# Kernel tuning notes

Hardware: AMD Instinct MI355X
Metric: run time of the kernel (lower is better)

## Reference

```python
import jax, jax.numpy as jnp
import numpy as np

B, C, N, K, COUT = 8, 128, 10000, 16, 256


def setup_inputs() -> dict:
    key = jax.random.key(0)
    ks = jax.random.split(key, 8)
    x = jax.random.normal(ks[0], (B, C, N, 1), dtype=jnp.float32)
    edge_index = jax.random.randint(ks[1], (2, B, N, K), 0, N)
    s1 = 1.0 / np.sqrt(C)
    W1 = jax.random.uniform(ks[2], (C, C), jnp.float32, -s1, s1)   # nn1 1x1 conv weight
    b1 = jax.random.uniform(ks[3], (C,), jnp.float32, -s1, s1)
    Wp = jax.random.uniform(ks[4], (C, C), jnp.float32, -s1, s1)   # nn_pooling Linear
    bp = jax.random.uniform(ks[5], (C,), jnp.float32, -s1, s1)
    s2 = 1.0 / np.sqrt(2 * C)
    W2 = jax.random.uniform(ks[6], (COUT, 2 * C), jnp.float32, -s2, s2)  # nn2 1x1 conv
    b2 = jax.random.uniform(ks[7], (COUT,), jnp.float32, -s2, s2)
    return dict(x=x, edge_index=edge_index, W1=W1, b1=b1, Wp=Wp, bp=bp, W2=W2, b2=b2)


def reference(x, edge_index, W1, b1, Wp, bp, W2, b2):
    b, c, n, _ = x.shape
    k = edge_index.shape[-1]
    # nn1: 1x1 conv (channel mix) + ReLU -> [B,C,N,1]
    h = jax.nn.relu(jnp.einsum('bcns,dc->bdns', x, W1) + b1[None, :, None, None])
    # batched_index_select: gather neighbor features along vertex dim -> [B,C,N,K]
    hn = h[:, :, :, 0]                              # [B,C,N]
    idx = edge_index[0].reshape(b, 1, n * k)        # broadcast over C
    xj = jnp.take_along_axis(hn, idx, axis=2).reshape(b, c, n, k)
    # nn_pooling: Linear over channel dim + ReLU (transpose(1,3) in torch == act on C)
    xj = jax.nn.relu(jnp.einsum('bcnk,dc->bdnk', xj, Wp) + bp[None, :, None, None])
    # max-pool over neighbors, keepdim -> [B,C,N,1]
    xj = jnp.max(xj, axis=-1, keepdims=True)
    # concat along channels, nn2: 1x1 conv + ReLU -> [B,COUT,N,1]
    cat = jnp.concatenate([h, xj], axis=1)
    out = jax.nn.relu(jnp.einsum('bcns,dc->bdns', cat, W2) + b2[None, :, None, None])
    return out
```

## Files before the change

### kernel.cpp

```cpp
#include <hip/hip_runtime.h>

#define NODES 10000
#define BATCH 8
#define CH    128
#define KNB   16
#define CO    256

typedef __bf16 bf16x8 __attribute__((ext_vector_type(8)));
typedef float  f32x4  __attribute__((ext_vector_type(4)));

__device__ __forceinline__ unsigned short f2bf(float f) {
  unsigned u = __float_as_uint(f);
  u = (u + 0x7FFFu + ((u >> 16) & 1u)) >> 16;
  return (unsigned short)u;
}

__device__ __forceinline__ unsigned pkmax(unsigned a, unsigned b) {
  unsigned d;
  asm("v_pk_max_u16 %0, %1, %2" : "=v"(d) : "v"(a), "v"(b));
  return d;
}
__device__ __forceinline__ uint4 pkmax4(uint4 a, uint4 b) {
  a.x = pkmax(a.x, b.x); a.y = pkmax(a.y, b.y);
  a.z = pkmax(a.z, b.z); a.w = pkmax(a.w, b.w);
  return a;
}
__device__ __forceinline__ bf16x8 asbf8(uint4 u) {
  union { uint4 u; bf16x8 b; } c; c.u = u; return c.b;
}

__device__ __forceinline__ void gload_lds16(const void* g, void* l) {
  __builtin_amdgcn_global_load_lds(
      (const __attribute__((address_space(1))) unsigned int*)g,
      (__attribute__((address_space(3))) unsigned int*)l, 16, 0, 0);
}

__device__ __forceinline__ void lds_barrier() {
  asm volatile("s_waitcnt lgkmcnt(0)" ::: "memory");
  __builtin_amdgcn_sched_barrier(0);
  __builtin_amdgcn_s_barrier();
}

__global__ __launch_bounds__(256) void prep(
    const float* __restrict__ W1, const float* __restrict__ Wp,
    const float* __restrict__ W2,
    unsigned short* __restrict__ W1b, unsigned short* __restrict__ Wpb,
    unsigned short* __restrict__ W2b)
{
  int i = blockIdx.x * 256 + threadIdx.x;
  const float* src; unsigned short* dst; int off;
  if (i < 4096)      { src = W1; dst = W1b; off = i; }
  else if (i < 8192) { src = Wp; dst = Wpb; off = i - 4096; }
  else               { src = W2; dst = W2b; off = i - 8192; }
  float4 v = ((const float4*)src)[off];
  ushort4 o;
  o.x = f2bf(v.x); o.y = f2bf(v.y); o.z = f2bf(v.z); o.w = f2bf(v.w);
  ((ushort4*)dst)[off] = o;
}

__device__ __forceinline__ void hz_load_x(
    f32x4 (&xa)[4][2], const float* __restrict__ X, int n0, int t)
{
#pragma unroll
  for (int rep = 0; rep < 4; ++rep) {
    int flat = t + rep * 256;
    int c2 = flat >> 4, n4 = flat & 15;
    int c  = c2 * 2;
    int gn = n0 + n4 * 4;
    f32x4 a0 = (f32x4){0.f,0.f,0.f,0.f}, a1 = a0;
    if (gn < NODES) {
      a0 = *(const f32x4*)(X + (size_t)c * NODES + gn);
      a1 = *(const f32x4*)(X + (size_t)(c + 1) * NODES + gn);
    }
    xa[rep][0] = a0; xa[rep][1] = a1;
  }
}

__device__ __forceinline__ void hz_write_buf(
    const f32x4 (&xa)[4][2], unsigned short* buf, int t)
{
  char* BtB = (char*)buf;
#pragma unroll
  for (int rep = 0; rep < 4; ++rep) {
    int flat = t + rep * 256;
    int c2 = flat >> 4, n4 = flat & 15;
#pragma unroll
    for (int i = 0; i < 4; ++i) {
      int nn = n4 * 4 + i;
      unsigned pk = (unsigned)f2bf(xa[rep][0][i])
                  | ((unsigned)f2bf(xa[rep][1][i]) << 16);
      int phys = nn * 256 + (((c2 >> 2) ^ (nn & 7)) << 4) + ((c2 & 3) << 2);
      *(unsigned*)(BtB + phys) = pk;
    }
  }
}

__device__ __forceinline__ void hz_compute(
    const unsigned short* buf, unsigned short* Ht, unsigned short* Zt,
    const uint4 (&af)[4][4], const uint4 (&af2)[4][4],
    const float* __restrict__ b1, const float* __restrict__ bp,
    unsigned short* __restrict__ h_t, unsigned short* __restrict__ z_t,
    size_t nb, int n0, int t, int w, int lm, int q)
{
  const char* BtB = (const char*)buf;
  char* HtB = (char*)Ht;
  char* ZtB = (char*)Zt;
  const int d0  = (w & 1) * 64;
  const int nbw = (w >> 1) * 32;

  f32x4 acc[4][2];
#pragma unroll
  for (int dt = 0; dt < 4; ++dt)
#pragma unroll
    for (int nt = 0; nt < 2; ++nt) acc[dt][nt] = (f32x4){0.f,0.f,0.f,0.f};

#pragma unroll
  for (int kt = 0; kt < 4; ++kt)
#pragma unroll
    for (int nt = 0; nt < 2; ++nt) {
      int nl = nbw + nt * 16 + lm;
      int chunk = kt * 4 + q;
      int phys = nl * 256 + ((chunk ^ (nl & 7)) << 4);
      bf16x8 bb = asbf8(*(const uint4*)(BtB + phys));
#pragma unroll
      for (int dt = 0; dt < 4; ++dt)
        acc[dt][nt] = __builtin_amdgcn_mfma_f32_16x16x32_bf16(
            asbf8(af[dt][kt]), bb, acc[dt][nt], 0, 0, 0);
    }

#pragma unroll
  for (int dt = 0; dt < 4; ++dt) {
    int dbase = d0 + dt * 16 + q * 4;
    float4 bi = *(const float4*)(b1 + dbase);
    float bv[4] = {bi.x, bi.y, bi.z, bi.w};
#pragma unroll
    for (int nt = 0; nt < 2; ++nt) {
      int nl = nbw + nt * 16 + lm;
      ushort4 o;
      o.x = f2bf(fmaxf(acc[dt][nt][0] + bv[0], 0.f));
      o.y = f2bf(fmaxf(acc[dt][nt][1] + bv[1], 0.f));
      o.z = f2bf(fmaxf(acc[dt][nt][2] + bv[2], 0.f));
      o.w = f2bf(fmaxf(acc[dt][nt][3] + bv[3], 0.f));
      int chunk = dbase >> 3;
      int phys  = nl * 256 + ((chunk ^ (nl & 7)) << 4) + ((q & 1) << 3);
      *(ushort4*)(HtB + phys) = o;
    }
  }

  lds_barrier();

  {
    int nl = t >> 2;
    int gn = n0 + nl;
#pragma unroll
    for (int rep = 0; rep < 4; ++rep) {
      int g = (t & 3) + rep * 4;
      int phys = nl * 256 + ((g ^ (nl & 7)) << 4);
      uint4 v = *(const uint4*)(HtB + phys);
      if (gn < NODES)
        *(uint4*)((char*)h_t + (nb + (size_t)gn) * 256 + g * 16) = v;
    }
  }

#pragma unroll
  for (int dt = 0; dt < 4; ++dt)
#pragma unroll
    for (int nt = 0; nt < 2; ++nt) acc[dt][nt] = (f32x4){0.f,0.f,0.f,0.f};

#pragma unroll
  for (int kt = 0; kt < 4; ++kt)
#pragma unroll
    for (int nt = 0; nt < 2; ++nt) {
      int nl = nbw + nt * 16 + lm;
      int chunk = kt * 4 + q;
      int phys = nl * 256 + ((chunk ^ (nl & 7)) << 4);
      bf16x8 bb = asbf8(*(const uint4*)(HtB + phys));
#pragma unroll
      for (int dt = 0; dt < 4; ++dt)
        acc[dt][nt] = __builtin_amdgcn_mfma_f32_16x16x32_bf16(
            asbf8(af2[dt][kt]), bb, acc[dt][nt], 0, 0, 0);
    }

#pragma unroll
  for (int dt = 0; dt < 4; ++dt) {
    int dbase = d0 + dt * 16 + q * 4;
    float4 bi = *(const float4*)(bp + dbase);
    float bv[4] = {bi.x, bi.y, bi.z, bi.w};
#pragma unroll
    for (int nt = 0; nt < 2; ++nt) {
      int nl = nbw + nt * 16 + lm;
      ushort4 o;
      o.x = f2bf(fmaxf(acc[dt][nt][0] + bv[0], 0.f));
      o.y = f2bf(fmaxf(acc[dt][nt][1] + bv[1], 0.f));
      o.z = f2bf(fmaxf(acc[dt][nt][2] + bv[2], 0.f));
      o.w = f2bf(fmaxf(acc[dt][nt][3] + bv[3], 0.f));
      int chunk = dbase >> 3;
      int phys  = nl * 256 + ((chunk ^ (nl & 7)) << 4) + ((q & 1) << 3);
      *(ushort4*)(ZtB + phys) = o;
    }
  }

  lds_barrier();

  {
    int nl = t >> 2;
    int gn = n0 + nl;
#pragma unroll
    for (int rep = 0; rep < 4; ++rep) {
      int g = (t & 3) + rep * 4;
      int phys = nl * 256 + ((g ^ (nl & 7)) << 4);
      uint4 v = *(const uint4*)(ZtB + phys);
      if (gn < NODES)
        *(uint4*)((char*)z_t + (nb + (size_t)gn) * 256 + g * 16) = v;
    }
  }
}

__global__ __launch_bounds__(256) void fused_hz(
    const unsigned short* __restrict__ W1b, const float* __restrict__ b1,
    const unsigned short* __restrict__ Wpb, const float* __restrict__ bp,
    const float* __restrict__ x,
    unsigned short* __restrict__ h_t, unsigned short* __restrict__ z_t)
{
  const int bid = blockIdx.x;
  const int b   = bid & 7;
  const int g   = bid >> 3;
  const int t   = threadIdx.x;
  const int lane = t & 63, w = t >> 6;
  const int lm = lane & 15, q = lane >> 4;
  const size_t nb = (size_t)b * NODES;
  const float* X = x + (size_t)b * CH * NODES;

  __shared__ __align__(16) unsigned short bufA[64 * 128];
  __shared__ __align__(16) unsigned short bufB[64 * 128];
  __shared__ __align__(16) unsigned short Ht[64 * 128];
  __shared__ __align__(16) unsigned short Zt[64 * 128];

  const int d0 = (w & 1) * 64;

  uint4 af[4][4], af2[4][4];
#pragma unroll
  for (int dt = 0; dt < 4; ++dt)
#pragma unroll
    for (int kt = 0; kt < 4; ++kt) {
      af[dt][kt]  = *(const uint4*)(W1b + (d0 + dt*16 + lm) * CH + kt*32 + q*8);
      af2[dt][kt] = *(const uint4*)(Wpb + (d0 + dt*16 + lm) * CH + kt*32 + q*8);
    }

  const int n0_0 = g * 64;
  const int n0_1 = (g + 64) * 64;
  const int n0_2 = (g + 128) * 64;
  const bool has2 = (g + 128) < 157;

  f32x4 xa[4][2];

  hz_load_x(xa, X, n0_0, t);
  hz_write_buf(xa, bufA, t);
  __syncthreads();

  hz_load_x(xa, X, n0_1, t);
  hz_compute(bufA, Ht, Zt, af, af2, b1, bp, h_t, z_t, nb, n0_0, t, w, lm, q);
  hz_write_buf(xa, bufB, t);
  __syncthreads();

  if (has2) {
    hz_load_x(xa, X, n0_2, t);
    hz_compute(bufB, Ht, Zt, af, af2, b1, bp, h_t, z_t, nb, n0_1, t, w, lm, q);
    hz_write_buf(xa, bufA, t);
    __syncthreads();
    hz_compute(bufA, Ht, Zt, af, af2, b1, bp, h_t, z_t, nb, n0_2, t, w, lm, q);
  } else {
    hz_compute(bufB, Ht, Zt, af, af2, b1, bp, h_t, z_t, nb, n0_1, t, w, lm, q);
  }
}

__global__ __launch_bounds__(256) void gmax_kernel(
    const unsigned short* __restrict__ z_t, const int* __restrict__ e0,
    unsigned short* __restrict__ zm)
{
  const int bid = blockIdx.x;
  const int b   = bid & 7;
  const int n0  = (bid >> 3) * 64;
  const int t   = threadIdx.x;
  const int nl  = t >> 2, c = t & 3;
  const int gn  = n0 + nl;
  if (gn >= NODES) return;

  const int* ip = e0 + ((size_t)b * NODES + gn) * KNB;
  int4 iv0 = *(const int4*)(ip);
  int4 iv1 = *(const int4*)(ip + 4);
  int4 iv2 = *(const int4*)(ip + 8);
  int4 iv3 = *(const int4*)(ip + 12);
  int idx[16] = {iv0.x, iv0.y, iv0.z, iv0.w,
                 iv1.x, iv1.y, iv1.z, iv1.w,
                 iv2.x, iv2.y, iv2.z, iv2.w,
                 iv3.x, iv3.y, iv3.z, iv3.w};

  const char* Z = (const char*)(z_t + (size_t)b * NODES * CH) + c * 16;
  uint4 m[4];
#pragma unroll
  for (int cg = 0; cg < 4; ++cg) m[cg] = make_uint4(0u, 0u, 0u, 0u);

#pragma unroll
  for (int k = 0; k < KNB; ++k) {
    const char* p = Z + (size_t)idx[k] * (CH * 2);
#pragma unroll
    for (int cg = 0; cg < 4; ++cg)
      m[cg] = pkmax4(m[cg], *(const uint4*)(p + cg * 64));
  }

  char* O = (char*)(zm + ((size_t)b * NODES + gn) * CH) + c * 16;
#pragma unroll
  for (int cg = 0; cg < 4; ++cg)
    *(uint4*)(O + cg * 64) = m[cg];
}

__device__ __forceinline__ void og_stage(
    unsigned short* buf, const unsigned short* __restrict__ h_t,
    const unsigned short* __restrict__ zm, size_t nb, int n0, int w, int lane)
{
#pragma unroll
  for (int rep = 0; rep < 8; ++rep) {
    const int row0 = w * 2 + rep * 8;
    const int nl = row0 + (lane >> 5);
    const int l  = (lane & 31) ^ (nl & 7);
    int gn = n0 + nl; if (gn > NODES - 1) gn = NODES - 1;
    const unsigned short* src = (l < 16)
        ? h_t + (nb + (size_t)gn) * CH + l * 8
        : zm  + (nb + (size_t)gn) * CH + (l - 16) * 8;
    gload_lds16(src, (char*)buf + row0 * 512);
  }
  __builtin_amdgcn_sched_barrier(0);
}

__device__ __forceinline__ void og_mfma(
    f32x4 (&acc)[4][4], const unsigned short* buf,
    const uint4 (&af)[8][4], int lm, int q)
{
  const char* catB = (const char*)buf;
#pragma unroll
  for (int dt = 0; dt < 4; ++dt)
#pragma unroll
    for (int nt = 0; nt < 4; ++nt) acc[dt][nt] = (f32x4){0.f, 0.f, 0.f, 0.f};
#pragma unroll
  for (int kt = 0; kt < 8; ++kt)
#pragma unroll
    for (int nt = 0; nt < 4; ++nt) {
      int nl = nt * 16 + lm;
      int chunk = kt * 4 + q;
      int phys = nl * 512 + ((chunk ^ (nl & 7)) << 4);
      bf16x8 bb = asbf8(*(const uint4*)(catB + phys));
#pragma unroll
      for (int dt = 0; dt < 4; ++dt)
        acc[dt][nt] = __builtin_amdgcn_mfma_f32_16x16x32_bf16(
            asbf8(af[kt][dt]), bb, acc[dt][nt], 0, 0, 0);
    }
}

__device__ __forceinline__ void og_epi(
    const f32x4 (&acc)[4][4], const float* __restrict__ b2,
    float* __restrict__ out, int b, int n0, int w, int lm, int q)
{
  const int d0 = w * 64;
#pragma unroll
  for (int dt = 0; dt < 4; ++dt) {
    int dbase = d0 + dt * 16 + q * 4;
    float4 bi = *(const float4*)(b2 + dbase);
    float bv[4] = {bi.x, bi.y, bi.z, bi.w};
#pragma unroll
    for (int nt = 0; nt < 4; ++nt) {
      int gn = n0 + nt * 16 + lm;
      if (gn < NODES) {
        float* op = out + ((size_t)(b * CO + dbase) * NODES) + gn;
#pragma unroll
        for (int r = 0; r < 4; ++r)
          op[(size_t)r * NODES] = fmaxf(acc[dt][nt][r] + bv[r], 0.f);
      }
    }
  }
}

__global__ __launch_bounds__(256) void out_gemm(
    const unsigned short* __restrict__ h_t, const unsigned short* __restrict__ zm,
    const unsigned short* __restrict__ W2b, const float* __restrict__ b2,
    float* __restrict__ out)
{
  const int bid = blockIdx.x;
  const int b   = bid & 7;
  const int g   = bid >> 3;
  const int t   = threadIdx.x;
  const int lane = t & 63, w = t >> 6;
  const int lm = lane & 15, q = lane >> 4;
  const size_t nb = (size_t)b * NODES;

  __shared__ __align__(16) unsigned short bufA[64 * 256];
  __shared__ __align__(16) unsigned short bufB[64 * 256];

  const int d0 = w * 64;
  uint4 af[8][4];
#pragma unroll
  for (int kt = 0; kt < 8; ++kt)
#pragma unroll
    for (int dt = 0; dt < 4; ++dt)
      af[kt][dt] = *(const uint4*)(W2b + (d0 + dt*16 + lm) * CO + kt*32 + q*8);

  const int n0_0 = g * 64;
  const int n0_1 = (g + 64) * 64;
  const int n0_2 = (g + 128) * 64;
  const bool has2 = (g + 128) < 157;

  f32x4 acc[4][4];

  og_stage(bufA, h_t, zm, nb, n0_0, w, lane);
  asm volatile("s_waitcnt vmcnt(0) lgkmcnt(0)" ::: "memory");
  __builtin_amdgcn_sched_barrier(0);
  __builtin_amdgcn_s_barrier();

  og_stage(bufB, h_t, zm, nb, n0_1, w, lane);
  og_mfma(acc, bufA, af, lm, q);
  asm volatile("s_waitcnt vmcnt(0) lgkmcnt(0)" ::: "memory");
  __builtin_amdgcn_sched_barrier(0);
  __builtin_amdgcn_s_barrier();

  if (has2) {
    og_stage(bufA, h_t, zm, nb, n0_2, w, lane);
    og_epi(acc, b2, out, b, n0_0, w, lm, q);
    og_mfma(acc, bufB, af, lm, q);
    asm volatile("s_waitcnt vmcnt(56) lgkmcnt(0)" ::: "memory");
    __builtin_amdgcn_sched_barrier(0);
    __builtin_amdgcn_s_barrier();
    og_epi(acc, b2, out, b, n0_1, w, lm, q);
    og_mfma(acc, bufA, af, lm, q);
    og_epi(acc, b2, out, b, n0_2, w, lm, q);
  } else {
    og_epi(acc, b2, out, b, n0_0, w, lm, q);
    og_mfma(acc, bufB, af, lm, q);
    og_epi(acc, b2, out, b, n0_1, w, lm, q);
  }
}

extern "C" void kernel_launch(void* const* d_in, const int* in_sizes, int n_in,
                              void* d_out, int out_size, void* d_ws, size_t ws_size,
                              hipStream_t stream) {
  const float* x  = (const float*)d_in[0];
  const int*   ei = (const int*)d_in[1];
  const float* W1 = (const float*)d_in[2];
  const float* b1 = (const float*)d_in[3];
  const float* Wp = (const float*)d_in[4];
  const float* bp = (const float*)d_in[5];
  const float* W2 = (const float*)d_in[6];
  const float* b2 = (const float*)d_in[7];
  float* out = (float*)d_out;

  unsigned short* ws  = (unsigned short*)d_ws;
  unsigned short* h_t = ws;
  unsigned short* z_t = h_t + (size_t)BATCH * NODES * CH;
  unsigned short* W1b = z_t + (size_t)BATCH * NODES * CH;
  unsigned short* Wpb = W1b + CH * CH;
  unsigned short* W2b = Wpb + CH * CH;
  unsigned short* zm  = W2b + CO * 2 * CH;

  prep<<<96, 256, 0, stream>>>(W1, Wp, W2, W1b, Wpb, W2b);

  const int NT = (NODES + 63) / 64;
  fused_hz<<<512, 256, 0, stream>>>(W1b, b1, Wpb, bp, x, h_t, z_t);
  gmax_kernel<<<BATCH * NT, 256, 0, stream>>>(z_t, ei, zm);
  out_gemm<<<512, 256, 0, stream>>>(h_t, zm, W2b, b2, out);
}
```

Measured before the change: 195.0 us.

## Split fused_hz into two-tile blocks and reuse input LDS buffer for Z staging

Each fused_hz block now handles two consecutive 64-node tiles instead of up to three strided tiles, and the grid grows to cover all tiles (8×79 blocks). The separate Zt shared buffer is dropped: the Z output is staged in the input tile buffer once it has been consumed, cutting shared memory per block from 64KB to 48KB. The goal is more resident blocks per CU and less serial work per block, improving latency hiding for the memory-bound first stage. In exchange, each block gets less software pipelining of x loads, and reusing the buffer depends on every wave having finished reading it before it is overwritten.

After: 201.7 us. 3.4% more time.

```diff
diff --git a/kernel.cpp b/kernel.cpp
--- a/kernel.cpp
+++ b/kernel.cpp
@@ -96,15 +96,15 @@
 }
 
 __device__ __forceinline__ void hz_compute(
-    const unsigned short* buf, unsigned short* Ht, unsigned short* Zt,
+    unsigned short* buf,
+    unsigned short* Ht,
     const uint4 (&af)[4][4], const uint4 (&af2)[4][4],
     const float* __restrict__ b1, const float* __restrict__ bp,
     unsigned short* __restrict__ h_t, unsigned short* __restrict__ z_t,
     size_t nb, int n0, int t, int w, int lm, int q)
 {
-  const char* BtB = (const char*)buf;
+  char* BtB = (char*)buf;
   char* HtB = (char*)Ht;
-  char* ZtB = (char*)Zt;
   const int d0  = (w & 1) * 64;
   const int nbw = (w >> 1) * 32;
 
@@ -196,7 +196,7 @@
       o.w = f2bf(fmaxf(acc[dt][nt][3] + bv[3], 0.f));
       int chunk = dbase >> 3;
       int phys  = nl * 256 + ((chunk ^ (nl & 7)) << 4) + ((q & 1) << 3);
-      *(ushort4*)(ZtB + phys) = o;
+      *(ushort4*)(BtB + phys) = o;
     }
   }
 
@@ -209,7 +209,7 @@
     for (int rep = 0; rep < 4; ++rep) {
       int g = (t & 3) + rep * 4;
       int phys = nl * 256 + ((g ^ (nl & 7)) << 4);
-      uint4 v = *(const uint4*)(ZtB + phys);
+      uint4 v = *(const uint4*)(BtB + phys);
       if (gn < NODES)
         *(uint4*)((char*)z_t + (nb + (size_t)gn) * 256 + g * 16) = v;
     }
@@ -224,7 +224,7 @@
 {
   const int bid = blockIdx.x;
   const int b   = bid & 7;
-  const int g   = bid >> 3;
+  const int p   = bid >> 3;
   const int t   = threadIdx.x;
   const int lane = t & 63, w = t >> 6;
   const int lm = lane & 15, q = lane >> 4;
@@ -234,7 +234,6 @@
   __shared__ __align__(16) unsigned short bufA[64 * 128];
   __shared__ __align__(16) unsigned short bufB[64 * 128];
   __shared__ __align__(16) unsigned short Ht[64 * 128];
-  __shared__ __align__(16) unsigned short Zt[64 * 128];
 
   const int d0 = (w & 1) * 64;
 
@@ -247,10 +246,9 @@
       af2[dt][kt] = *(const uint4*)(Wpb + (d0 + dt*16 + lm) * CH + kt*32 + q*8);
     }
 
-  const int n0_0 = g * 64;
-  const int n0_1 = (g + 64) * 64;
-  const int n0_2 = (g + 128) * 64;
-  const bool has2 = (g + 128) < 157;
+  const int n0_0 = p * 128;
+  const int n0_1 = n0_0 + 64;
+  const bool has1 = n0_1 < NODES;
 
   f32x4 xa[4][2];
 
@@ -258,19 +256,14 @@
   hz_write_buf(xa, bufA, t);
   __syncthreads();
 
-  hz_load_x(xa, X, n0_1, t);
-  hz_compute(bufA, Ht, Zt, af, af2, b1, bp, h_t, z_t, nb, n0_0, t, w, lm, q);
-  hz_write_buf(xa, bufB, t);
-  __syncthreads();
-
-  if (has2) {
-    hz_load_x(xa, X, n0_2, t);
-    hz_compute(bufB, Ht, Zt, af, af2, b1, bp, h_t, z_t, nb, n0_1, t, w, lm, q);
-    hz_write_buf(xa, bufA, t);
+  if (has1) {
+    hz_load_x(xa, X, n0_1, t);
+    hz_compute(bufA, Ht, af, af2, b1, bp, h_t, z_t, nb, n0_0, t, w, lm, q);
+    hz_write_buf(xa, bufB, t);
     __syncthreads();
-    hz_compute(bufA, Ht, Zt, af, af2, b1, bp, h_t, z_t, nb, n0_2, t, w, lm, q);
+    hz_compute(bufB, Ht, af, af2, b1, bp, h_t, z_t, nb, n0_1, t, w, lm, q);
   } else {
-    hz_compute(bufB, Ht, Zt, af, af2, b1, bp, h_t, z_t, nb, n0_1, t, w, lm, q);
+    hz_compute(bufA, Ht, af, af2, b1, bp, h_t, z_t, nb, n0_0, t, w, lm, q);
   }
 }
 
@@ -463,7 +456,8 @@
   prep<<<96, 256, 0, stream>>>(W1, Wp, W2, W1b, Wpb, W2b);
 
   const int NT = (NODES + 63) / 64;
-  fused_hz<<<512, 256, 0, stream>>>(W1b, b1, Wpb, bp, x, h_t, z_t);
+  const int NP = (NT + 1) / 2;
+  fused_hz<<<BATCH * NP, 256, 0, stream>>>(W1b, b1, Wpb, bp, x, h_t, z_t);
   gmax_kernel<<<BATCH * NT, 256, 0, stream>>>(z_t, ei, zm);
   out_gemm<<<512, 256, 0, stream>>>(h_t, zm, W2b, b2, out);
 }
```
